# Optimization experiments

Hardware: AMD Instinct MI355X
Metric: run time of the kernel (lower is better)

Reference implementation:

```python
import jax, jax.numpy as jnp
import numpy as np

N = 100000      # nodes
E = 1600000     # edges
NF, EF = 8, 4   # raw node/edge feature dims
HID = 64        # hidden_dim
HEADS = 4
C = HID // HEADS  # per-head channels = 16
L = 3           # num_layers
NEG_SLOPE = 0.2 # PyG GATConv leaky_relu slope
LN_EPS = 1e-5


def setup_inputs():
    key = jax.random.key(0)
    ks = jax.random.split(key, 16)
    s = 0.1
    return {
        "x": jax.random.normal(ks[0], (N, NF), dtype=jnp.float32),
        "edge_index": jax.random.randint(ks[1], (2, E), 0, N, dtype=jnp.int32),
        "edge_attr": jax.random.normal(ks[2], (E, EF), dtype=jnp.float32),
        "node_w": jax.random.normal(ks[3], (NF, HID), dtype=jnp.float32) * s,
        "node_b": jnp.zeros((HID,), jnp.float32),
        "edge_w": jax.random.normal(ks[4], (EF, HID), dtype=jnp.float32) * s,
        "edge_b": jnp.zeros((HID,), jnp.float32),
        "lin_w": jax.random.normal(ks[5], (L, HID, HEADS * C), dtype=jnp.float32) * s,
        "lin_edge_w": jax.random.normal(ks[6], (L, HID, HEADS * C), dtype=jnp.float32) * s,
        "att_src": jax.random.normal(ks[7], (L, HEADS, C), dtype=jnp.float32) * s,
        "att_dst": jax.random.normal(ks[8], (L, HEADS, C), dtype=jnp.float32) * s,
        "att_edge": jax.random.normal(ks[9], (L, HEADS, C), dtype=jnp.float32) * s,
        "gat_bias": jnp.zeros((L, HID), jnp.float32),
        "ln_gamma": jnp.ones((L, HID), jnp.float32),
        "ln_beta": jnp.zeros((L, HID), jnp.float32),
    }


def _layer_norm(x, g, b):
    mu = jnp.mean(x, axis=-1, keepdims=True)
    var = jnp.mean(jnp.square(x - mu), axis=-1, keepdims=True)
    return (x - mu) * jax.lax.rsqrt(var + LN_EPS) * g + b


def _gat_conv(x, src, dst, e_proj, lin_w, lin_edge_w, a_src_w, a_dst_w, a_edge_w, bias):
    """PyG GATConv (concat=True, edge_dim, self-loops with fill='mean').
    x: [N,HID]; src/dst: [E'] (already include self loops); e_proj: [E',HID]."""
    n = x.shape[0]
    xs = (x @ lin_w).reshape(n, HEADS, C)                    # [N,H,C]
    ea = (e_proj @ lin_edge_w).reshape(-1, HEADS, C)         # [E',H,C]
    a_src = jnp.einsum('nhc,hc->nh', xs, a_src_w)            # [N,H]
    a_dst = jnp.einsum('nhc,hc->nh', xs, a_dst_w)            # [N,H]
    a_edge = jnp.einsum('ehc,hc->eh', ea, a_edge_w)          # [E',H]
    alpha = a_src[src] + a_dst[dst] + a_edge                 # [E',H]
    alpha = jax.nn.leaky_relu(alpha, NEG_SLOPE)
    # segment softmax over edges sharing a destination node
    amax = jax.ops.segment_max(alpha, dst, num_segments=n)   # [N,H]
    ex = jnp.exp(alpha - amax[dst])
    denom = jax.ops.segment_sum(ex, dst, num_segments=n)     # [N,H]
    w = ex / (denom[dst] + 1e-16)                            # [E',H]
    msg = xs[src] * w[:, :, None]                            # [E',H,C]
    out = jax.ops.segment_sum(msg, dst, num_segments=n)      # [N,H,C]
    return out.reshape(n, HEADS * C) + bias


def reference(x, edge_index, edge_attr, node_w, node_b, edge_w, edge_b,
              lin_w, lin_edge_w, att_src, att_dst, att_edge, gat_bias,
              ln_gamma, ln_beta):
    h = x @ node_w + node_b                                  # [N,HID]
    e = edge_attr @ edge_w + edge_b                          # [E,HID]
    src, dst = edge_index[0], edge_index[1]
    # add self loops once (same for all layers); edge_attr fill = per-dst mean
    ones = jnp.ones((E,), h.dtype)
    deg = jax.ops.segment_sum(ones, dst, num_segments=N)     # [N]
    e_mean = jax.ops.segment_sum(e, dst, num_segments=N) / jnp.maximum(deg, 1.0)[:, None]
    loop = jnp.arange(N, dtype=src.dtype)
    src_f = jnp.concatenate([src, loop])
    dst_f = jnp.concatenate([dst, loop])
    e_f = jnp.concatenate([e, e_mean], axis=0)               # [E+N,HID]
    for i in range(L):
        residual = h
        h = _gat_conv(h, src_f, dst_f, e_f, lin_w[i], lin_edge_w[i],
                      att_src[i], att_dst[i], att_edge[i], gat_bias[i])
        h = _layer_norm(h + residual, ln_gamma[i], ln_beta[i])
        h = jax.nn.relu(h)
    return h
```

## Files before the change

### kernel.cpp

```cpp
#include <hip/hip_runtime.h>


#define LRELU_SLOPE 0.2f
#define LOG2E 1.4426950408889634f
#define P1B 512
#define NBKT_MAX 512

typedef float f32x2 __attribute__((ext_vector_type(2)));

#ifdef __has_builtin
#if __has_builtin(__builtin_amdgcn_fdot2_f32_bf16)
#define HAS_BF16DOT 1
#endif
#endif
#ifndef HAS_BF16DOT
#define HAS_BF16DOT 0
#endif

#if HAS_BF16DOT
typedef __bf16 bf16x2_t __attribute__((ext_vector_type(2)));
#endif

__device__ __forceinline__ f32x2 fp8lo(unsigned int v) {
    return __builtin_amdgcn_cvt_pk_f32_fp8((int)v, false);
}
__device__ __forceinline__ f32x2 fp8hi(unsigned int v) {
    return __builtin_amdgcn_cvt_pk_f32_fp8((int)v, true);
}
__device__ __forceinline__ ushort f2bf(float x) {
    unsigned int b = __float_as_uint(x);
    return (ushort)((b + 0x7fffu + ((b >> 16) & 1u)) >> 16);
}
__device__ __forceinline__ unsigned int pack2bf(float a, float b) {
    return (unsigned int)f2bf(a) | ((unsigned int)f2bf(b) << 16);
}
__device__ __forceinline__ float bf_lo(unsigned int v) { return __uint_as_float(v << 16); }
__device__ __forceinline__ float bf_hi(unsigned int v) { return __uint_as_float(v & 0xffff0000u); }

__device__ __forceinline__ float dot2bf(unsigned int a, unsigned int b, float c) {
#if HAS_BF16DOT
    return __builtin_amdgcn_fdot2_f32_bf16(__builtin_bit_cast(bf16x2_t, a),
                                           __builtin_bit_cast(bf16x2_t, b), c, false);
#else
    return fmaf(bf_lo(a), bf_lo(b), fmaf(bf_hi(a), bf_hi(b), c));
#endif
}

__global__ void k_smallw(const float* __restrict__ lin_edge_w,
                         const float* __restrict__ att_edge,
                         const float* __restrict__ edge_w,
                         const float* __restrict__ edge_b,
                         float* __restrict__ Mc)
{
    __shared__ float we[3][64][4];
    int t = threadIdx.x;
    if (t < 192) {
        int l = t >> 6, k = t & 63;
        for (int h = 0; h < 4; ++h) {
            float acc = 0.f;
            #pragma unroll
            for (int c = 0; c < 16; ++c)
                acc = fmaf(lin_edge_w[l*4096 + k*64 + h*16 + c],
                           att_edge[l*64 + h*16 + c], acc);
            we[l][k][h] = acc;
        }
    }
    __syncthreads();
    if (t < 48) {
        int l = t >> 4, k4 = (t >> 2) & 3, h = t & 3;
        float acc = 0.f;
        for (int k = 0; k < 64; ++k)
            acc = fmaf(edge_w[k4*64 + k], we[l][k][h], acc);
        Mc[l*16 + k4*4 + h] = acc * LOG2E;
    }
    if (t >= 64 && t < 76) {
        int u = t - 64, l = u >> 2, h = u & 3;
        float acc = 0.f;
        for (int k = 0; k < 64; ++k)
            acc = fmaf(edge_b[k], we[l][k][h], acc);
        Mc[48 + l*4 + h] = acc * LOG2E;
    }
}

__global__ void k_node_proj(const float* __restrict__ x, const float* __restrict__ nw,
                            const float* __restrict__ nb, ushort* __restrict__ hbf,
                            int n_nodes)
{
    int idx = blockIdx.x * blockDim.x + threadIdx.x;
    int n = idx >> 6, j = idx & 63;
    if (n >= n_nodes) return;
    float acc = nb[j];
    #pragma unroll
    for (int k = 0; k < 8; ++k) acc = fmaf(x[n*8 + k], nw[k*64 + j], acc);
    hbf[(size_t)n*64 + j] = f2bf(acc);
}

__global__ __launch_bounds__(256) void k_hist1(const int* __restrict__ dst,
                                               int* __restrict__ C,
                                               int E, int chunk, int nbkt) {
    __shared__ int h[NBKT_MAX];
    int b = blockIdx.x, t = threadIdx.x;
    for (int i = t; i < nbkt; i += 256) h[i] = 0;
    __syncthreads();
    int e0 = b*chunk, e1 = min(e0 + chunk, E);
    for (int e = e0 + t; e < e1; e += 256)
        atomicAdd(&h[dst[e] >> 8], 1);
    __syncthreads();
    for (int i = t; i < nbkt; i += 256) C[i*P1B + b] = h[i];
}

__global__ void k_scanA(const int* __restrict__ in, int* __restrict__ out,
                        int* __restrict__ bsum, int n) {
    __shared__ int s[1024];
    int i = blockIdx.x*1024 + threadIdx.x;
    s[threadIdx.x] = (i < n) ? in[i] : 0;
    __syncthreads();
    for (int off = 1; off < 1024; off <<= 1) {
        int t = (threadIdx.x >= off) ? s[threadIdx.x - off] : 0;
        __syncthreads();
        s[threadIdx.x] += t;
        __syncthreads();
    }
    if (i < n) out[i] = s[threadIdx.x];
    if (threadIdx.x == 1023) bsum[blockIdx.x] = s[1023];
}

__global__ void k_scanB(int* bsum, int nb) {
    __shared__ int s[1024];
    int t = threadIdx.x;
    int own = (t < nb) ? bsum[t] : 0;
    s[t] = own;
    __syncthreads();
    for (int off = 1; off < 1024; off <<= 1) {
        int v = (t >= off) ? s[t - off] : 0;
        __syncthreads();
        s[t] += v;
        __syncthreads();
    }
    if (t < nb) bsum[t] = s[t] - own;
}

__global__ void k_scanC(int* __restrict__ S, const int* __restrict__ bsum, int n) {
    int i = blockIdx.x*1024 + threadIdx.x;
    if (i < n) S[i] += bsum[blockIdx.x];
}

__global__ __launch_bounds__(256) void k_scat1(const int* __restrict__ dst,
        const int* __restrict__ srcv, const float4* __restrict__ ea,
        const int* __restrict__ S, uint2* __restrict__ brec,
        int E, int chunk, int nbkt) {
    __shared__ int base[NBKT_MAX];
    __shared__ int cur[NBKT_MAX];
    int b = blockIdx.x, t = threadIdx.x;
    for (int i = t; i < nbkt; i += 256) {
        int flat = i*P1B + b;
        base[i] = flat ? S[flat - 1] : 0;
        cur[i] = 0;
    }
    __syncthreads();
    int e0 = b*chunk, e1 = min(e0 + chunk, E);
    for (int e = e0 + t; e < e1; e += 256) {
        int d = dst[e];
        int bin = d >> 8;
        int lr = atomicAdd(&cur[bin], 1);
        int slot = base[bin] + lr;
        float4 v = ea[e];
        unsigned int p = (unsigned int)__builtin_amdgcn_cvt_pk_fp8_f32(v.x, v.y, 0, false);
        p = (unsigned int)__builtin_amdgcn_cvt_pk_fp8_f32(v.z, v.w, (int)p, true);
        uint2 r;
        r.x = (unsigned int)srcv[e] | ((unsigned int)(d & 255) << 24);
        r.y = p;
        brec[slot] = r;
    }
}

__global__ __launch_bounds__(256) void k_csr(const uint2* __restrict__ brec,
        const int* __restrict__ S, uint2* __restrict__ recs,
        int* __restrict__ rowptr, int nbkt, int NN, int E) {
    int bkt = blockIdx.x, t = threadIdx.x;
    __shared__ int cnt[256], exc[256], cur[256], ssc[256];
    int seg_b = bkt ? S[bkt*P1B - 1] : 0;
    int seg_e = S[(bkt + 1)*P1B - 1];
    cnt[t] = 0; cur[t] = 0;
    __syncthreads();
    for (int i = seg_b + t; i < seg_e; i += 256)
        atomicAdd(&cnt[brec[i].x >> 24], 1);
    __syncthreads();
    ssc[t] = cnt[t];
    __syncthreads();
    for (int off = 1; off < 256; off <<= 1) {
        int v = (t >= off) ? ssc[t - off] : 0;
        __syncthreads();
        ssc[t] += v;
        __syncthreads();
    }
    exc[t] = ssc[t] - cnt[t];
    __syncthreads();
    int g = bkt*256 + t;
    if (g < NN) rowptr[g] = seg_b + exc[t];
    if (bkt == nbkt - 1 && t == 0) rowptr[NN] = E;
    for (int i = seg_b + t; i < seg_e; i += 256) {
        uint2 r = brec[i];
        int dl = (int)(r.x >> 24);
        int slot = seg_b + exc[dl] + atomicAdd(&cur[dl], 1);
        r.x &= 0x00FFFFFFu;
        recs[slot] = r;
    }
}

__global__ void k_eamean(const int* __restrict__ rowptr, const uint2* __restrict__ recs,
                         float4* __restrict__ ea_mean, int n) {
    int i = blockIdx.x*blockDim.x + threadIdx.x;
    if (i >= n) return;
    int b = rowptr[i], e = rowptr[i + 1];
    float sx = 0.f, sy = 0.f, sz = 0.f, sw = 0.f;
    for (int s = b; s < e; ++s) {
        unsigned int p = recs[s].y;
        f32x2 lo = fp8lo(p), hi = fp8hi(p);
        sx += lo.x; sy += lo.y; sz += hi.x; sw += hi.y;
    }
    float inv = (e > b) ? 1.f / (float)(e - b) : 0.f;
    ea_mean[i] = make_float4(sx*inv, sy*inv, sz*inv, sw*inv);
}

__global__ __launch_bounds__(256) void k_proj(const ushort* __restrict__ hbf,
        const float* __restrict__ lw,
        const float* __restrict__ asw,
        const float* __restrict__ adw,
        ushort* __restrict__ xs2, float* __restrict__ a_src4,
        float* __restrict__ a_dst4, int n_nodes)
{
    __shared__ unsigned int Wp[2048];
    for (int i = threadIdx.x; i < 2048; i += 256) {
        int k2 = i >> 6, c = i & 63;
        Wp[i] = pack2bf(lw[(k2*2)*64 + c], lw[(k2*2+1)*64 + c]);
    }
    __syncthreads();
    int lane = threadIdx.x & 63, wid = threadIdx.x >> 6;
    float as_w = asw[lane] * LOG2E, ad_w = adw[lane] * LOG2E;
    int nquads = (n_nodes + 3) >> 2;
    int nlast = n_nodes - 1;
    for (int q = blockIdx.x*4 + wid; q < nquads; q += gridDim.x*4) {
        int n0 = q << 2;
        int n1 = min(n0+1, nlast), n2 = min(n0+2, nlast), n3 = min(n0+3, nlast);
        const uint4* r0p = (const uint4*)(hbf + (size_t)n0*64);
        const uint4* r1p = (const uint4*)(hbf + (size_t)n1*64);
        const uint4* r2p = (const uint4*)(hbf + (size_t)n2*64);
        const uint4* r3p = (const uint4*)(hbf + (size_t)n3*64);
        float acc0 = 0.f, acc1 = 0.f, acc2 = 0.f, acc3 = 0.f;
        #pragma unroll
        for (int qq = 0; qq < 8; ++qq) {
            uint4 u0 = r0p[qq], u1 = r1p[qq], u2 = r2p[qq], u3 = r3p[qq];
            unsigned int w0 = Wp[(qq*4+0)*64 + lane];
            unsigned int w1 = Wp[(qq*4+1)*64 + lane];
            unsigned int w2 = Wp[(qq*4+2)*64 + lane];
            unsigned int w3 = Wp[(qq*4+3)*64 + lane];
            acc0 = dot2bf(u0.w, w3, dot2bf(u0.z, w2, dot2bf(u0.y, w1, dot2bf(u0.x, w0, acc0))));
            acc1 = dot2bf(u1.w, w3, dot2bf(u1.z, w2, dot2bf(u1.y, w1, dot2bf(u1.x, w0, acc1))));
            acc2 = dot2bf(u2.w, w3, dot2bf(u2.z, w2, dot2bf(u2.y, w1, dot2bf(u2.x, w0, acc2))));
            acc3 = dot2bf(u3.w, w3, dot2bf(u3.z, w2, dot2bf(u3.y, w1, dot2bf(u3.x, w0, acc3))));
        }
        xs2[(size_t)n0*64 + lane] = f2bf(acc0);
        xs2[(size_t)n1*64 + lane] = f2bf(acc1);
        xs2[(size_t)n2*64 + lane] = f2bf(acc2);
        xs2[(size_t)n3*64 + lane] = f2bf(acc3);
        #define ARED(ACC, NJ) { \
            float ps = (ACC)*as_w, pd = (ACC)*ad_w; \
            ps += __shfl_xor(ps,1,16); pd += __shfl_xor(pd,1,16); \
            ps += __shfl_xor(ps,2,16); pd += __shfl_xor(pd,2,16); \
            ps += __shfl_xor(ps,4,16); pd += __shfl_xor(pd,4,16); \
            ps += __shfl_xor(ps,8,16); pd += __shfl_xor(pd,8,16); \
            if ((lane & 15) == 0) { \
                a_src4[(NJ)*4 + (lane>>4)] = ps; \
                a_dst4[(NJ)*4 + (lane>>4)] = pd; \
            } }
        ARED(acc0, n0) ARED(acc1, n1) ARED(acc2, n2) ARED(acc3, n3)
        #undef ARED
    }
}

__global__ __launch_bounds__(256) void k_gat(const uint4* __restrict__ xs4,
        const float* __restrict__ a_src4, const float* __restrict__ a_dst4,
        const int* __restrict__ rowptr, const uint2* __restrict__ recs,
        const float4* __restrict__ ea_mean,
        const float* __restrict__ Mc,
        const float* __restrict__ c0,
        const float* __restrict__ bias, const float* __restrict__ lng,
        const float* __restrict__ lnb,
        const ushort* __restrict__ hbf_in, ushort* __restrict__ hbf_out,
        float* __restrict__ out_f32, int last, int n_nodes)
{
    int n = blockIdx.x*4 + (threadIdx.x >> 6);
    if (n >= n_nodes) return;
    int lane = threadIdx.x & 63;
    int k8  = lane & 7;
    int hB  = k8 >> 1;
    int grp = lane >> 3;
    int cb = k8 * 8;
    uint4 rr = *(const uint4*)(hbf_in + (size_t)n*64 + cb);
    float4 eam = ea_mean[n];
    float m0 = Mc[hB], m1 = Mc[4+hB], m2 = Mc[8+hB], m3 = Mc[12+hB];
    float c0v = c0[hB];
    float adv = a_dst4[n*4 + hB];
    float cc = c0v + adv;
    int rb = rowptr[n], re = rowptr[n + 1];

    float denL = 0.f;
    float a0=0.f,a1=0.f,a2=0.f,a3=0.f,a4=0.f,a5=0.f,a6=0.f,a7=0.f;

    if (rb < re) {
        int last_e = re - 1;
        int i0 = rb + grp;     i0 = (i0 > last_e) ? last_e : i0;
        uint2 rc = recs[i0];
        int i1 = rb + 8 + grp; i1 = (i1 > last_e) ? last_e : i1;
        uint2 rn = recs[i1];
        float asc = a_src4[(int)rc.x*4 + hB];
        uint4 xc = xs4[(unsigned)rc.x*8u + (unsigned)k8];
        #pragma unroll 2
        for (int b = rb; b < re; b += 8) {
            int i2 = b + 16 + grp; i2 = (i2 > last_e) ? last_e : i2;
            uint2 r2 = recs[i2];
            float asn = a_src4[(int)rn.x*4 + hB];
            uint4 xn = xs4[(unsigned)rn.x*8u + (unsigned)k8];
            f32x2 e01 = fp8lo(rc.y), e23 = fp8hi(rc.y);
            float al = fmaf(e01.x, m0, fmaf(e01.y, m1,
                       fmaf(e23.x, m2, fmaf(e23.y, m3, cc)))) + asc;
            al = fmaxf(al, LRELU_SLOPE * al);
            float ev = (b + grp < re) ? exp2f(al) : 0.f;
            denL += ev;
            a0 = fmaf(bf_lo(xc.x), ev, a0); a1 = fmaf(bf_hi(xc.x), ev, a1);
            a2 = fmaf(bf_lo(xc.y), ev, a2); a3 = fmaf(bf_hi(xc.y), ev, a3);
            a4 = fmaf(bf_lo(xc.z), ev, a4); a5 = fmaf(bf_hi(xc.z), ev, a5);
            a6 = fmaf(bf_lo(xc.w), ev, a6); a7 = fmaf(bf_hi(xc.w), ev, a7);
            rc = rn; rn = r2; asc = asn; xc = xn;
        }
    }
    denL += __shfl_xor(denL, 8); denL += __shfl_xor(denL, 16); denL += __shfl_xor(denL, 32);
    #define XR(A) A += __shfl_xor(A, 8); A += __shfl_xor(A, 16); A += __shfl_xor(A, 32);
    XR(a0) XR(a1) XR(a2) XR(a3) XR(a4) XR(a5) XR(a6) XR(a7)
    #undef XR
    float ael = (re > rb)
        ? fmaf(eam.x, m0, fmaf(eam.y, m1, fmaf(eam.z, m2, fmaf(eam.w, m3, c0v))))
        : 0.f;
    float alS = a_src4[n*4 + hB] + adv + ael;
    alS = fmaxf(alS, LRELU_SLOPE * alS);
    float evS = exp2f(alS);
    float denF = denL + evS;
    uint4 vs = xs4[(unsigned)n*8u + (unsigned)k8];
    a0 = fmaf(bf_lo(vs.x), evS, a0); a1 = fmaf(bf_hi(vs.x), evS, a1);
    a2 = fmaf(bf_lo(vs.y), evS, a2); a3 = fmaf(bf_hi(vs.y), evS, a3);
    a4 = fmaf(bf_lo(vs.z), evS, a4); a5 = fmaf(bf_hi(vs.z), evS, a5);
    a6 = fmaf(bf_lo(vs.w), evS, a6); a7 = fmaf(bf_hi(vs.w), evS, a7);
    float inv = 1.f / (denF + 1e-16f);
    const float4* bp = (const float4*)(bias + cb);
    float4 b0 = bp[0], b1 = bp[1];
    float o0 = a0*inv + b0.x + bf_lo(rr.x), o1 = a1*inv + b0.y + bf_hi(rr.x);
    float o2 = a2*inv + b0.z + bf_lo(rr.y), o3 = a3*inv + b0.w + bf_hi(rr.y);
    float o4 = a4*inv + b1.x + bf_lo(rr.z), o5 = a5*inv + b1.y + bf_hi(rr.z);
    float o6 = a6*inv + b1.z + bf_lo(rr.w), o7 = a7*inv + b1.w + bf_hi(rr.w);
    float s1 = o0+o1+o2+o3+o4+o5+o6+o7;
    s1 += __shfl_xor(s1, 1); s1 += __shfl_xor(s1, 2); s1 += __shfl_xor(s1, 4);
    float mu = s1 * 0.015625f;
    float d0=o0-mu,d1=o1-mu,d2=o2-mu,d3=o3-mu,d4=o4-mu,d5=o5-mu,d6=o6-mu,d7=o7-mu;
    float s2 = d0*d0+d1*d1+d2*d2+d3*d3+d4*d4+d5*d5+d6*d6+d7*d7;
    s2 += __shfl_xor(s2, 1); s2 += __shfl_xor(s2, 2); s2 += __shfl_xor(s2, 4);
    float rs = rsqrtf(s2 * 0.015625f + 1e-5f);
    const float4* gp = (const float4*)(lng + cb);
    const float4* zp = (const float4*)(lnb + cb);
    float4 g0 = gp[0], g1 = gp[1], z0 = zp[0], z1 = zp[1];
    float y0 = fmaxf(d0*rs*g0.x + z0.x, 0.f), y1 = fmaxf(d1*rs*g0.y + z0.y, 0.f);
    float y2 = fmaxf(d2*rs*g0.z + z0.z, 0.f), y3 = fmaxf(d3*rs*g0.w + z0.w, 0.f);
    float y4 = fmaxf(d4*rs*g1.x + z1.x, 0.f), y5 = fmaxf(d5*rs*g1.y + z1.y, 0.f);
    float y6 = fmaxf(d6*rs*g1.z + z1.z, 0.f), y7 = fmaxf(d7*rs*g1.w + z1.w, 0.f);
    if (lane < 8) {
        if (last) {
            float4* outp = (float4*)(out_f32 + (size_t)n*64 + cb);
            outp[0] = make_float4(y0, y1, y2, y3);
            outp[1] = make_float4(y4, y5, y6, y7);
        } else {
            uint4 pk;
            pk.x = pack2bf(y0, y1); pk.y = pack2bf(y2, y3);
            pk.z = pack2bf(y4, y5); pk.w = pack2bf(y6, y7);
            *(uint4*)(hbf_out + (size_t)n*64 + cb) = pk;
        }
    }
}

extern "C" void kernel_launch(void* const* d_in, const int* in_sizes, int n_in,
                              void* d_out, int out_size, void* d_ws, size_t ws_size,
                              hipStream_t stream) {
    const float* x          = (const float*)d_in[0];
    const int*   ei         = (const int*)d_in[1];
    const float* edge_attr  = (const float*)d_in[2];
    const float* node_w     = (const float*)d_in[3];
    const float* node_b     = (const float*)d_in[4];
    const float* edge_w     = (const float*)d_in[5];
    const float* edge_b     = (const float*)d_in[6];
    const float* lin_w      = (const float*)d_in[7];
    const float* lin_edge_w = (const float*)d_in[8];
    const float* att_src    = (const float*)d_in[9];
    const float* att_dst    = (const float*)d_in[10];
    const float* att_edge   = (const float*)d_in[11];
    const float* gat_bias   = (const float*)d_in[12];
    const float* ln_g       = (const float*)d_in[13];
    const float* ln_b       = (const float*)d_in[14];

    int NN = in_sizes[0] / 8;
    int E  = in_sizes[1] / 2;
    const int* src = ei;
    const int* dst = ei + E;

    int nbkt = (NN + 255) >> 8;
    int ntot = nbkt * P1B;
    int chunk = (E + P1B - 1) / P1B;

    char* wsp = (char*)d_ws;
    size_t off = 0;
    auto alloc = [&](size_t bytes) -> void* {
        off = (off + 255) & ~(size_t)255;
        void* p = wsp + off;
        off += bytes;
        return p;
    };
    ushort* h_bf    = (ushort*)alloc((size_t)NN * 64 * 2);
    ushort* xs2     = (ushort*)alloc((size_t)NN * 64 * 2);
    float*  a_src4  = (float*)alloc((size_t)NN * 4 * 4);
    float*  a_dst4  = (float*)alloc((size_t)NN * 4 * 4);
    uint2*  recs    = (uint2*)alloc((size_t)E * 8);
    uint2*  brec    = (uint2*)alloc((size_t)E * 8);
    float4* ea_mean = (float4*)alloc((size_t)NN * 16);
    int*    rowptr  = (int*)alloc((size_t)(NN + 1) * 4);
    int*    S       = (int*)alloc((size_t)ntot * 4);
    int*    bsum    = (int*)alloc(4096);
    float*  Mc      = (float*)alloc(256);

    k_smallw<<<1, 256, 0, stream>>>(lin_edge_w, att_edge, edge_w, edge_b, Mc);
    k_node_proj<<<(NN*64 + 255) / 256, 256, 0, stream>>>(x, node_w, node_b, h_bf, NN);
    k_hist1<<<P1B, 256, 0, stream>>>(dst, S, E, chunk, nbkt);
    int nsb = (ntot + 1023) / 1024;
    k_scanA<<<nsb, 1024, 0, stream>>>(S, S, bsum, ntot);
    k_scanB<<<1, 1024, 0, stream>>>(bsum, nsb);
    k_scanC<<<nsb, 1024, 0, stream>>>(S, bsum, ntot);
    k_scat1<<<P1B, 256, 0, stream>>>(dst, src, (const float4*)edge_attr,
                                     S, brec, E, chunk, nbkt);
    k_csr<<<nbkt, 256, 0, stream>>>(brec, S, recs, rowptr, nbkt, NN, E);
    k_eamean<<<(NN + 255) / 256, 256, 0, stream>>>(rowptr, recs, ea_mean, NN);

    for (int l = 0; l < 3; ++l) {
        k_proj<<<2048, 256, 0, stream>>>(h_bf, lin_w + l*4096, att_src + l*64,
                                         att_dst + l*64, xs2, a_src4, a_dst4, NN);
        k_gat<<<(NN + 3) / 4, 256, 0, stream>>>((const uint4*)xs2, a_src4, a_dst4,
                                                rowptr, recs, ea_mean,
                                                Mc + l*16, Mc + 48 + l*4,
                                                gat_bias + l*64, ln_g + l*64, ln_b + l*64,
                                                h_bf, h_bf, (float*)d_out,
                                                (l == 2) ? 1 : 0, NN);
    }
}
```

Measured before the change: 376.1 us.

## Process one node per 8-lane group with degree-sorted node permutation

The GAT aggregation kernel now gives each destination node to an 8-lane group that walks its edges serially. Before, a full wavefront served one node, with 8 edge groups reduced by cross-lane shuffles. The CSR build now also emits a per-bucket permutation that orders nodes by in-degree, so the nodes sharing a wavefront have similar edge counts and lanes stay balanced. Separately, the weight-precompute and node-projection kernels are merged into one launch, and the scan fix-up kernel is removed by adding block sums at read time. The goal is to remove shuffle reductions and idle lanes. The cost is a longer serial loop per node with a shallower prefetch distance, and scattered node access through the permutation.

Result: no change. 375.8 us (-0.1%).

```diff
diff --git a/kernel.cpp b/kernel.cpp
--- a/kernel.cpp
+++ b/kernel.cpp
@@ -46,47 +46,47 @@
 #endif
 }
 
-__global__ void k_smallw(const float* __restrict__ lin_edge_w,
-                         const float* __restrict__ att_edge,
-                         const float* __restrict__ edge_w,
-                         const float* __restrict__ edge_b,
-                         float* __restrict__ Mc)
+__global__ void k_prep0(const float* __restrict__ lin_edge_w,
+                        const float* __restrict__ att_edge,
+                        const float* __restrict__ edge_w,
+                        const float* __restrict__ edge_b,
+                        float* __restrict__ Mc,
+                        const float* __restrict__ x, const float* __restrict__ nw,
+                        const float* __restrict__ nb, ushort* __restrict__ hbf,
+                        int n_nodes)
 {
     __shared__ float we[3][64][4];
     int t = threadIdx.x;
-    if (t < 192) {
-        int l = t >> 6, k = t & 63;
-        for (int h = 0; h < 4; ++h) {
+    if (blockIdx.x == 0) {
+        if (t < 192) {
+            int l = t >> 6, k = t & 63;
+            for (int h = 0; h < 4; ++h) {
+                float acc = 0.f;
+                #pragma unroll
+                for (int c = 0; c < 16; ++c)
+                    acc = fmaf(lin_edge_w[l*4096 + k*64 + h*16 + c],
+                               att_edge[l*64 + h*16 + c], acc);
+                we[l][k][h] = acc;
+            }
+        }
+        __syncthreads();
+        if (t < 48) {
+            int l = t >> 4, k4 = (t >> 2) & 3, h = t & 3;
             float acc = 0.f;
-            #pragma unroll
-            for (int c = 0; c < 16; ++c)
-                acc = fmaf(lin_edge_w[l*4096 + k*64 + h*16 + c],
-                           att_edge[l*64 + h*16 + c], acc);
-            we[l][k][h] = acc;
-        }
-    }
-    __syncthreads();
-    if (t < 48) {
-        int l = t >> 4, k4 = (t >> 2) & 3, h = t & 3;
-        float acc = 0.f;
-        for (int k = 0; k < 64; ++k)
-            acc = fmaf(edge_w[k4*64 + k], we[l][k][h], acc);
-        Mc[l*16 + k4*4 + h] = acc * LOG2E;
-    }
-    if (t >= 64 && t < 76) {
-        int u = t - 64, l = u >> 2, h = u & 3;
-        float acc = 0.f;
-        for (int k = 0; k < 64; ++k)
-            acc = fmaf(edge_b[k], we[l][k][h], acc);
-        Mc[48 + l*4 + h] = acc * LOG2E;
-    }
-}
-
-__global__ void k_node_proj(const float* __restrict__ x, const float* __restrict__ nw,
-                            const float* __restrict__ nb, ushort* __restrict__ hbf,
-                            int n_nodes)
-{
-    int idx = blockIdx.x * blockDim.x + threadIdx.x;
+            for (int k = 0; k < 64; ++k)
+                acc = fmaf(edge_w[k4*64 + k], we[l][k][h], acc);
+            Mc[l*16 + k4*4 + h] = acc * LOG2E;
+        }
+        if (t >= 64 && t < 76) {
+            int u = t - 64, l = u >> 2, h = u & 3;
+            float acc = 0.f;
+            for (int k = 0; k < 64; ++k)
+                acc = fmaf(edge_b[k], we[l][k][h], acc);
+            Mc[48 + l*4 + h] = acc * LOG2E;
+        }
+        return;
+    }
+    int idx = (blockIdx.x - 1) * blockDim.x + t;
     int n = idx >> 6, j = idx & 63;
     if (n >= n_nodes) return;
     float acc = nb[j];
@@ -140,21 +140,20 @@
     if (t < nb) bsum[t] = s[t] - own;
 }
 
-__global__ void k_scanC(int* __restrict__ S, const int* __restrict__ bsum, int n) {
-    int i = blockIdx.x*1024 + threadIdx.x;
-    if (i < n) S[i] += bsum[blockIdx.x];
+__device__ __forceinline__ int scanned(const int* S, const int* bsum, int idx) {
+    return S[idx] + bsum[idx >> 10];
 }
 
 __global__ __launch_bounds__(256) void k_scat1(const int* __restrict__ dst,
         const int* __restrict__ srcv, const float4* __restrict__ ea,
-        const int* __restrict__ S, uint2* __restrict__ brec,
-        int E, int chunk, int nbkt) {
+        const int* __restrict__ S, const int* __restrict__ bsum,
+        uint2* __restrict__ brec, int E, int chunk, int nbkt) {
     __shared__ int base[NBKT_MAX];
     __shared__ int cur[NBKT_MAX];
     int b = blockIdx.x, t = threadIdx.x;
     for (int i = t; i < nbkt; i += 256) {
         int flat = i*P1B + b;
-        base[i] = flat ? S[flat - 1] : 0;
+        base[i] = flat ? scanned(S, bsum, flat - 1) : 0;
         cur[i] = 0;
     }
     __syncthreads();
@@ -175,13 +174,17 @@
 }
 
 __global__ __launch_bounds__(256) void k_csr(const uint2* __restrict__ brec,
-        const int* __restrict__ S, uint2* __restrict__ recs,
-        int* __restrict__ rowptr, int nbkt, int NN, int E) {
+        const int* __restrict__ S, const int* __restrict__ bsum,
+        uint2* __restrict__ recs, int* __restrict__ rowptr, int* __restrict__ perm,
+        int nbkt, int NN, int E) {
     int bkt = blockIdx.x, t = threadIdx.x;
     __shared__ int cnt[256], exc[256], cur[256], ssc[256];
-    int seg_b = bkt ? S[bkt*P1B - 1] : 0;
-    int seg_e = S[(bkt + 1)*P1B - 1];
+    __shared__ int dh[64], dsc[64], dcu[64];
+    int ib = bkt*P1B - 1, ie = (bkt + 1)*P1B - 1;
+    int seg_b = bkt ? scanned(S, bsum, ib) : 0;
+    int seg_e = scanned(S, bsum, ie);
     cnt[t] = 0; cur[t] = 0;
+    if (t < 64) { dh[t] = 0; dcu[t] = 0; }
     __syncthreads();
     for (int i = seg_b + t; i < seg_e; i += 256)
         atomicAdd(&cnt[brec[i].x >> 24], 1);
@@ -197,8 +200,24 @@
     exc[t] = ssc[t] - cnt[t];
     __syncthreads();
     int g = bkt*256 + t;
-    if (g < NN) rowptr[g] = seg_b + exc[t];
+    bool valid = (g < NN);
+    if (valid) rowptr[g] = seg_b + exc[t];
     if (bkt == nbkt - 1 && t == 0) rowptr[NN] = E;
+    int dcl = valid ? min(cnt[t], 63) : 0;
+    if (valid) atomicAdd(&dh[dcl], 1);
+    __syncthreads();
+    if (t < 64) dsc[t] = dh[t];
+    __syncthreads();
+    for (int off = 1; off < 64; off <<= 1) {
+        int v = (t >= off && t < 64) ? dsc[t - off] : 0;
+        __syncthreads();
+        if (t < 64) dsc[t] += v;
+        __syncthreads();
+    }
+    if (valid) {
+        int slot = (dsc[dcl] - dh[dcl]) + atomicAdd(&dcu[dcl], 1);
+        perm[bkt*256 + slot] = g;
+    }
     for (int i = seg_b + t; i < seg_e; i += 256) {
         uint2 r = brec[i];
         int dl = (int)(r.x >> 24);
@@ -282,7 +301,7 @@
 __global__ __launch_bounds__(256) void k_gat(const uint4* __restrict__ xs4,
         const float* __restrict__ a_src4, const float* __restrict__ a_dst4,
         const int* __restrict__ rowptr, const uint2* __restrict__ recs,
-        const float4* __restrict__ ea_mean,
+        const float4* __restrict__ ea_mean, const int* __restrict__ perm,
         const float* __restrict__ Mc,
         const float* __restrict__ c0,
         const float* __restrict__ bias, const float* __restrict__ lng,
@@ -290,43 +309,43 @@
         const ushort* __restrict__ hbf_in, ushort* __restrict__ hbf_out,
         float* __restrict__ out_f32, int last, int n_nodes)
 {
-    int n = blockIdx.x*4 + (threadIdx.x >> 6);
-    if (n >= n_nodes) return;
     int lane = threadIdx.x & 63;
-    int k8  = lane & 7;
-    int hB  = k8 >> 1;
-    int grp = lane >> 3;
-    int cb = k8 * 8;
+    int g8 = lane >> 3;
+    int gq = blockIdx.x*32 + (threadIdx.x >> 6)*8 + g8;
+    bool active = (gq < n_nodes);
+    int n = active ? perm[gq] : 0;
+    int oct = lane & 7;
+    int hB  = oct >> 1;
+    int cb = oct * 8;
     uint4 rr = *(const uint4*)(hbf_in + (size_t)n*64 + cb);
     float4 eam = ea_mean[n];
     float m0 = Mc[hB], m1 = Mc[4+hB], m2 = Mc[8+hB], m3 = Mc[12+hB];
     float c0v = c0[hB];
     float adv = a_dst4[n*4 + hB];
     float cc = c0v + adv;
-    int rb = rowptr[n], re = rowptr[n + 1];
+    int rb = rowptr[n], re = active ? rowptr[n + 1] : rb;
 
     float denL = 0.f;
     float a0=0.f,a1=0.f,a2=0.f,a3=0.f,a4=0.f,a5=0.f,a6=0.f,a7=0.f;
 
     if (rb < re) {
         int last_e = re - 1;
-        int i0 = rb + grp;     i0 = (i0 > last_e) ? last_e : i0;
-        uint2 rc = recs[i0];
-        int i1 = rb + 8 + grp; i1 = (i1 > last_e) ? last_e : i1;
+        uint2 rc = recs[rb];
+        int i1 = min(rb + 1, last_e);
         uint2 rn = recs[i1];
         float asc = a_src4[(int)rc.x*4 + hB];
-        uint4 xc = xs4[(unsigned)rc.x*8u + (unsigned)k8];
+        uint4 xc = xs4[(unsigned)rc.x*8u + (unsigned)oct];
         #pragma unroll 2
-        for (int b = rb; b < re; b += 8) {
-            int i2 = b + 16 + grp; i2 = (i2 > last_e) ? last_e : i2;
+        for (int b = rb; b < re; ++b) {
+            int i2 = min(b + 2, last_e);
             uint2 r2 = recs[i2];
             float asn = a_src4[(int)rn.x*4 + hB];
-            uint4 xn = xs4[(unsigned)rn.x*8u + (unsigned)k8];
+            uint4 xn = xs4[(unsigned)rn.x*8u + (unsigned)oct];
             f32x2 e01 = fp8lo(rc.y), e23 = fp8hi(rc.y);
             float al = fmaf(e01.x, m0, fmaf(e01.y, m1,
                        fmaf(e23.x, m2, fmaf(e23.y, m3, cc)))) + asc;
             al = fmaxf(al, LRELU_SLOPE * al);
-            float ev = (b + grp < re) ? exp2f(al) : 0.f;
+            float ev = exp2f(al);
             denL += ev;
             a0 = fmaf(bf_lo(xc.x), ev, a0); a1 = fmaf(bf_hi(xc.x), ev, a1);
             a2 = fmaf(bf_lo(xc.y), ev, a2); a3 = fmaf(bf_hi(xc.y), ev, a3);
@@ -335,10 +354,6 @@
             rc = rn; rn = r2; asc = asn; xc = xn;
         }
     }
-    denL += __shfl_xor(denL, 8); denL += __shfl_xor(denL, 16); denL += __shfl_xor(denL, 32);
-    #define XR(A) A += __shfl_xor(A, 8); A += __shfl_xor(A, 16); A += __shfl_xor(A, 32);
-    XR(a0) XR(a1) XR(a2) XR(a3) XR(a4) XR(a5) XR(a6) XR(a7)
-    #undef XR
     float ael = (re > rb)
         ? fmaf(eam.x, m0, fmaf(eam.y, m1, fmaf(eam.z, m2, fmaf(eam.w, m3, c0v))))
         : 0.f;
@@ -346,7 +361,7 @@
     alS = fmaxf(alS, LRELU_SLOPE * alS);
     float evS = exp2f(alS);
     float denF = denL + evS;
-    uint4 vs = xs4[(unsigned)n*8u + (unsigned)k8];
+    uint4 vs = xs4[(unsigned)n*8u + (unsigned)oct];
     a0 = fmaf(bf_lo(vs.x), evS, a0); a1 = fmaf(bf_hi(vs.x), evS, a1);
     a2 = fmaf(bf_lo(vs.y), evS, a2); a3 = fmaf(bf_hi(vs.y), evS, a3);
     a4 = fmaf(bf_lo(vs.z), evS, a4); a5 = fmaf(bf_hi(vs.z), evS, a5);
@@ -372,7 +387,7 @@
     float y2 = fmaxf(d2*rs*g0.z + z0.z, 0.f), y3 = fmaxf(d3*rs*g0.w + z0.w, 0.f);
     float y4 = fmaxf(d4*rs*g1.x + z1.x, 0.f), y5 = fmaxf(d5*rs*g1.y + z1.y, 0.f);
     float y6 = fmaxf(d6*rs*g1.z + z1.z, 0.f), y7 = fmaxf(d7*rs*g1.w + z1.w, 0.f);
-    if (lane < 8) {
+    if (active) {
         if (last) {
             float4* outp = (float4*)(out_f32 + (size_t)n*64 + cb);
             outp[0] = make_float4(y0, y1, y2, y3);
@@ -430,30 +445,30 @@
     uint2*  brec    = (uint2*)alloc((size_t)E * 8);
     float4* ea_mean = (float4*)alloc((size_t)NN * 16);
     int*    rowptr  = (int*)alloc((size_t)(NN + 1) * 4);
+    int*    perm    = (int*)alloc((size_t)NN * 4);
     int*    S       = (int*)alloc((size_t)ntot * 4);
     int*    bsum    = (int*)alloc(4096);
     float*  Mc      = (float*)alloc(256);
 
-    k_smallw<<<1, 256, 0, stream>>>(lin_edge_w, att_edge, edge_w, edge_b, Mc);
-    k_node_proj<<<(NN*64 + 255) / 256, 256, 0, stream>>>(x, node_w, node_b, h_bf, NN);
+    k_prep0<<<1 + (NN*64 + 255) / 256, 256, 0, stream>>>(
+        lin_edge_w, att_edge, edge_w, edge_b, Mc, x, node_w, node_b, h_bf, NN);
     k_hist1<<<P1B, 256, 0, stream>>>(dst, S, E, chunk, nbkt);
     int nsb = (ntot + 1023) / 1024;
     k_scanA<<<nsb, 1024, 0, stream>>>(S, S, bsum, ntot);
     k_scanB<<<1, 1024, 0, stream>>>(bsum, nsb);
-    k_scanC<<<nsb, 1024, 0, stream>>>(S, bsum, ntot);
     k_scat1<<<P1B, 256, 0, stream>>>(dst, src, (const float4*)edge_attr,
-                                     S, brec, E, chunk, nbkt);
-    k_csr<<<nbkt, 256, 0, stream>>>(brec, S, recs, rowptr, nbkt, NN, E);
+                                     S, bsum, brec, E, chunk, nbkt);
+    k_csr<<<nbkt, 256, 0, stream>>>(brec, S, bsum, recs, rowptr, perm, nbkt, NN, E);
     k_eamean<<<(NN + 255) / 256, 256, 0, stream>>>(rowptr, recs, ea_mean, NN);
 
     for (int l = 0; l < 3; ++l) {
         k_proj<<<2048, 256, 0, stream>>>(h_bf, lin_w + l*4096, att_src + l*64,
                                          att_dst + l*64, xs2, a_src4, a_dst4, NN);
-        k_gat<<<(NN + 3) / 4, 256, 0, stream>>>((const uint4*)xs2, a_src4, a_dst4,
-                                                rowptr, recs, ea_mean,
-                                                Mc + l*16, Mc + 48 + l*4,
-                                                gat_bias + l*64, ln_g + l*64, ln_b + l*64,
-                                                h_bf, h_bf, (float*)d_out,
-                                                (l == 2) ? 1 : 0, NN);
-    }
-}
+        k_gat<<<(NN + 31) / 32, 256, 0, stream>>>((const uint4*)xs2, a_src4, a_dst4,
+                                                  rowptr, recs, ea_mean, perm,
+                                                  Mc + l*16, Mc + 48 + l*4,
+                                                  gat_bias + l*64, ln_g + l*64, ln_b + l*64,
+                                                  h_bf, h_bf, (float*)d_out,
+                                                  (l == 2) ? 1 : 0, NN);
+    }
+}
```
